# Kernel optimization log

Measured on AMD Instinct MI355X. Metric: run time of the kernel, lower is better.

Reference implementation:

```python
import jax, jax.numpy as jnp
import numpy as np

ANCHOR_RADIUS = 5.0


def setup_inputs() -> dict:
    key = jax.random.key(0)
    k1, k2, k3 = jax.random.split(key, 3)
    B, N, E, S = 4, 1024, 32, 2
    embedding = jax.random.normal(k1, (B, N, E), dtype=jnp.float32)
    abs_coords = 10.0 * jax.random.normal(k2, (B, N, S), dtype=jnp.float32)
    patch_mask = jax.random.bernoulli(k3, 0.5, (B, N, N))  # bool [B,N,N]
    return {"embedding": embedding, "abs_coords": abs_coords, "patch_mask": patch_mask}


def reference(embedding, abs_coords, patch_mask):
    B, N, E = embedding.shape
    # pairwise coordinate and embedding differences
    coord_diff = abs_coords[:, :, None, :] - abs_coords[:, None, :, :]   # [B,N,N,2]
    diff = embedding[:, :, None, :] - embedding[:, None, :, :]           # [B,N,N,E]
    diff = diff.at[..., :2].add(coord_diff)
    ssq = jnp.sum(diff * diff, axis=-1)                                   # [B,N,N]
    # safe sqrt: zero grad at zero distance (matches torch norm subgradient)
    dist = jnp.where(ssq == 0, 0.0, jnp.sqrt(jnp.where(ssq == 0, 1.0, ssq)))
    sim = 1.0 - jax.nn.sigmoid(dist * 5.0 / ANCHOR_RADIUS - 5.0)          # [B,N,N]

    # negatives: sim with positive-pair mask and diagonal set to -inf
    eye = jnp.eye(N, dtype=bool)
    neg_mask = patch_mask | eye
    neg_masked = jnp.where(neg_mask, -jnp.inf, sim)                       # [B,N,N]
    lse_neg = jax.scipy.special.logsumexp(neg_masked, axis=-1)            # [B,N]

    # For each positive pair (b,i,j) with patch_mask[b,i,j]:
    #   logits = [sim[b,i,j], neg_masked[b,i,:]] ; CE target=0 ->
    #   loss_contrib = logaddexp(sim[b,i,j], lse_neg[b,i]) - sim[b,i,j]
    lse_tot = jnp.logaddexp(sim, lse_neg[:, :, None])                     # [B,N,N]
    loss = jnp.sum(jnp.where(patch_mask, lse_tot - sim, 0.0))
    return loss
```

## Files before the change

### kernel.cpp

```cpp
#include <hip/hip_runtime.h>

#define BBATCH 4
#define NN 1024
#define EE 32

typedef short v8s __attribute__((ext_vector_type(8)));
typedef float v4f __attribute__((ext_vector_type(4)));

__device__ __forceinline__ unsigned short f32_to_bf16(float v) {
    unsigned u = __builtin_bit_cast(unsigned, v);
    u += 0x7fffu + ((u >> 16) & 1u);
    return (unsigned short)(u >> 16);
}

__global__ __launch_bounds__(1024) void fused_kernel(
    const float* __restrict__ emb, const float* __restrict__ coords,
    const int* __restrict__ mask, float* __restrict__ out)
{
    const int bid = blockIdx.x;
    const int is = bid & 63;
    const int b  = bid >> 6;
    const int tid  = threadIdx.x;
    const int wave = tid >> 6, lane = tid & 63;
    const int m = lane & 15, q = lane >> 4;

    __shared__ unsigned short yh_s[NN * EE];
    __shared__ float nrm_s[NN];
    __shared__ float sums_w[16][16];
    __shared__ float total_s[16];
    __shared__ float wred[16];

    const float4* src4 = (const float4*)(emb + (size_t)b * NN * EE);
    const float*  crdb = coords + (size_t)b * NN * 2;
    #pragma unroll
    for (int w = 0; w < 8; ++w) {
        const int g  = w * 1024 + tid;
        const int r  = g >> 3, qq = g & 7;
        float4 v = src4[g];
        if (qq == 0) { v.x += crdb[r * 2 + 0]; v.y += crdb[r * 2 + 1]; }
        ushort4 h;
        h.x = f32_to_bf16(v.x); h.y = f32_to_bf16(v.y);
        h.z = f32_to_bf16(v.z); h.w = f32_to_bf16(v.w);
        ((ushort4*)yh_s)[r * 8 + (qq ^ (r & 7))] = h;
        float p = v.x * v.x + v.y * v.y + v.z * v.z + v.w * v.w;
        #pragma unroll
        for (int off = 1; off < 8; off <<= 1) p += __shfl_xor(p, off, 64);
        if (qq == 0) nrm_s[r] = p;
    }
    __syncthreads();

    const int i0 = is * 16;
    const v8s af = *(const v8s*)(yh_s + ((i0 + m) * EE) + ((q ^ (m & 7)) * 8));
    float ni[4];
    #pragma unroll
    for (int r = 0; r < 4; ++r) ni[r] = nrm_s[i0 + q * 4 + r];

    const int jbase = wave * 64;
    float    ex[4][4];
    float    s[4] = {0.f, 0.f, 0.f, 0.f};
    unsigned mbits = 0u;

    #pragma unroll
    for (int t = 0; t < 4; ++t) {
        const int j0 = jbase + t * 16;
        const v8s bf = *(const v8s*)(yh_s + ((j0 + m) * EE) + ((q ^ (m & 7)) * 8));
        const float njv = nrm_s[j0 + m];
        int mk[4];
        #pragma unroll
        for (int r = 0; r < 4; ++r)
            mk[r] = mask[((size_t)(b * NN + i0 + q * 4 + r) << 10) + j0 + m];
        v4f d = __builtin_amdgcn_mfma_f32_16x16x32_bf16(af, bf, (v4f){0,0,0,0}, 0, 0, 0);
        #pragma unroll
        for (int r = 0; r < 4; ++r) {
            float ssq  = fmaxf(ni[r] + njv - 2.f * d[r], 0.f);
            float dist = sqrtf(ssq);
            float sm   = 1.f / (1.f + __expf(dist - 5.f));
            const float e = __expf(mk[r] != 0 ? -sm : sm);
            ex[t][r] = e;
            bool negm = (mk[r] != 0) || (i0 + q * 4 + r == j0 + m);
            s[r] += negm ? 0.f : e;
            if (mk[r] != 0) mbits |= 1u << (t * 4 + r);
        }
    }

    #pragma unroll
    for (int r = 0; r < 4; ++r) {
        float v = s[r];
        #pragma unroll
        for (int off = 8; off > 0; off >>= 1) v += __shfl_down(v, off, 16);
        if (m == 0) sums_w[wave][q * 4 + r] = v;
    }
    __syncthreads();
    if (tid < 16) {
        float tot = 0.f;
        #pragma unroll
        for (int w = 0; w < 16; ++w) tot += sums_w[w][tid];
        total_s[tid] = tot;
    }
    __syncthreads();

    float tot[4];
    #pragma unroll
    for (int r = 0; r < 4; ++r) tot[r] = total_s[q * 4 + r];
    float acc = 0.f;
    #pragma unroll
    for (int t = 0; t < 4; ++t)
        #pragma unroll
        for (int r = 0; r < 4; ++r)
            if ((mbits >> (t * 4 + r)) & 1u)
                acc += __logf(fmaf(tot[r], ex[t][r], 1.f));

    #pragma unroll
    for (int off = 32; off > 0; off >>= 1) acc += __shfl_down(acc, off, 64);
    if (lane == 0) wred[wave] = acc;
    __syncthreads();
    if (tid == 0) {
        float a = 0.f;
        #pragma unroll
        for (int w = 0; w < 16; ++w) a += wred[w];
        atomicAdd(out, a);
    }
}

extern "C" void kernel_launch(void* const* d_in, const int* in_sizes, int n_in,
                              void* d_out, int out_size, void* d_ws, size_t ws_size,
                              hipStream_t stream) {
    const float* emb    = (const float*)d_in[0];
    const float* coords = (const float*)d_in[1];
    const int*   mask   = (const int*)d_in[2];
    float*       out    = (float*)d_out;

    hipMemsetAsync(out, 0, sizeof(float), stream);
    fused_kernel<<<BBATCH * (NN / 16), 1024, 0, stream>>>(emb, coords, mask, out);
}
```

Before: 80.13 us.

## Hoist bf16 conversion and norms into a separate prep kernel

Moves the per-block conversion of embeddings (plus coords) to bf16 and the row-norm computation into a standalone prep kernel writing to workspace, so it is done once per batch instead of once per block. The main kernel now reads bf16 rows and norms directly from global memory and no longer needs 64KB of LDS or a block-wide barrier before compute. Also uses native sqrt/rcp intrinsics and a branchless masked log accumulation. Adds a second kernel launch and global-memory reads of the operands in place of LDS reads.

```diff
diff --git a/kernel.cpp b/kernel.cpp
--- a/kernel.cpp
+++ b/kernel.cpp
@@ -13,8 +13,26 @@
     return (unsigned short)(u >> 16);
 }
 
+__global__ __launch_bounds__(256) void prep_kernel(
+    const float* __restrict__ emb, const float* __restrict__ coords,
+    unsigned short* __restrict__ ybf, float* __restrict__ nrm)
+{
+    const int g  = blockIdx.x * 256 + threadIdx.x;
+    const int r  = g >> 3, qq = g & 7;
+    float4 v = ((const float4*)emb)[g];
+    if (qq == 0) { v.x += coords[r * 2 + 0]; v.y += coords[r * 2 + 1]; }
+    ushort4 h;
+    h.x = f32_to_bf16(v.x); h.y = f32_to_bf16(v.y);
+    h.z = f32_to_bf16(v.z); h.w = f32_to_bf16(v.w);
+    ((ushort4*)ybf)[g] = h;
+    float p = v.x * v.x + v.y * v.y + v.z * v.z + v.w * v.w;
+    #pragma unroll
+    for (int off = 1; off < 8; off <<= 1) p += __shfl_xor(p, off, 64);
+    if (qq == 0) nrm[r] = p;
+}
+
 __global__ __launch_bounds__(1024) void fused_kernel(
-    const float* __restrict__ emb, const float* __restrict__ coords,
+    const unsigned short* __restrict__ ybf, const float* __restrict__ nrm,
     const int* __restrict__ mask, float* __restrict__ out)
 {
     const int bid = blockIdx.x;
@@ -24,36 +42,19 @@
     const int wave = tid >> 6, lane = tid & 63;
     const int m = lane & 15, q = lane >> 4;
 
-    __shared__ unsigned short yh_s[NN * EE];
-    __shared__ float nrm_s[NN];
     __shared__ float sums_w[16][16];
     __shared__ float total_s[16];
     __shared__ float wred[16];
 
-    const float4* src4 = (const float4*)(emb + (size_t)b * NN * EE);
-    const float*  crdb = coords + (size_t)b * NN * 2;
-    #pragma unroll
-    for (int w = 0; w < 8; ++w) {
-        const int g  = w * 1024 + tid;
-        const int r  = g >> 3, qq = g & 7;
-        float4 v = src4[g];
-        if (qq == 0) { v.x += crdb[r * 2 + 0]; v.y += crdb[r * 2 + 1]; }
-        ushort4 h;
-        h.x = f32_to_bf16(v.x); h.y = f32_to_bf16(v.y);
-        h.z = f32_to_bf16(v.z); h.w = f32_to_bf16(v.w);
-        ((ushort4*)yh_s)[r * 8 + (qq ^ (r & 7))] = h;
-        float p = v.x * v.x + v.y * v.y + v.z * v.z + v.w * v.w;
-        #pragma unroll
-        for (int off = 1; off < 8; off <<= 1) p += __shfl_xor(p, off, 64);
-        if (qq == 0) nrm_s[r] = p;
-    }
-    __syncthreads();
+    const unsigned short* Y  = ybf + (size_t)b * NN * EE;
+    const float*          NR = nrm + b * NN;
+    const int i0   = is * 16;
+    const int irow = i0 + q * 4;
 
-    const int i0 = is * 16;
-    const v8s af = *(const v8s*)(yh_s + ((i0 + m) * EE) + ((q ^ (m & 7)) * 8));
+    const v8s af = *(const v8s*)(Y + (i0 + m) * EE + q * 8);
     float ni[4];
     #pragma unroll
-    for (int r = 0; r < 4; ++r) ni[r] = nrm_s[i0 + q * 4 + r];
+    for (int r = 0; r < 4; ++r) ni[r] = NR[irow + r];
 
     const int jbase = wave * 64;
     float    ex[4][4];
@@ -63,21 +64,22 @@
     #pragma unroll
     for (int t = 0; t < 4; ++t) {
         const int j0 = jbase + t * 16;
-        const v8s bf = *(const v8s*)(yh_s + ((j0 + m) * EE) + ((q ^ (m & 7)) * 8));
-        const float njv = nrm_s[j0 + m];
+        const v8s bfv = *(const v8s*)(Y + (j0 + m) * EE + q * 8);
+        const float njv = NR[j0 + m];
         int mk[4];
         #pragma unroll
         for (int r = 0; r < 4; ++r)
-            mk[r] = mask[((size_t)(b * NN + i0 + q * 4 + r) << 10) + j0 + m];
-        v4f d = __builtin_amdgcn_mfma_f32_16x16x32_bf16(af, bf, (v4f){0,0,0,0}, 0, 0, 0);
+            mk[r] = mask[((size_t)(b * NN + irow + r) << 10) + j0 + m];
+        v4f d = __builtin_amdgcn_mfma_f32_16x16x32_bf16(af, bfv, (v4f){0,0,0,0}, 0, 0, 0);
         #pragma unroll
         for (int r = 0; r < 4; ++r) {
-            float ssq  = fmaxf(ni[r] + njv - 2.f * d[r], 0.f);
-            float dist = sqrtf(ssq);
-            float sm   = 1.f / (1.f + __expf(dist - 5.f));
+            float nn   = ni[r] + njv;
+            float ssq  = fmaxf(fmaf(-2.f, d[r], nn), 0.f);
+            float dist = __builtin_amdgcn_sqrtf(ssq);
+            float sm   = __builtin_amdgcn_rcpf(1.f + __expf(dist - 5.f));
             const float e = __expf(mk[r] != 0 ? -sm : sm);
             ex[t][r] = e;
-            bool negm = (mk[r] != 0) || (i0 + q * 4 + r == j0 + m);
+            bool negm = (mk[r] != 0) || (irow + r == j0 + m);
             s[r] += negm ? 0.f : e;
             if (mk[r] != 0) mbits |= 1u << (t * 4 + r);
         }
@@ -106,9 +108,10 @@
     #pragma unroll
     for (int t = 0; t < 4; ++t)
         #pragma unroll
-        for (int r = 0; r < 4; ++r)
-            if ((mbits >> (t * 4 + r)) & 1u)
-                acc += __logf(fmaf(tot[r], ex[t][r], 1.f));
+        for (int r = 0; r < 4; ++r) {
+            float lg = __logf(fmaf(tot[r], ex[t][r], 1.f));
+            acc += ((mbits >> (t * 4 + r)) & 1u) ? lg : 0.f;
+        }
 
     #pragma unroll
     for (int off = 32; off > 0; off >>= 1) acc += __shfl_down(acc, off, 64);
@@ -130,6 +133,10 @@
     const int*   mask   = (const int*)d_in[2];
     float*       out    = (float*)d_out;
 
+    unsigned short* ybf = (unsigned short*)d_ws;
+    float*          nrv = (float*)((char*)d_ws + BBATCH * NN * EE * 2);
+
     hipMemsetAsync(out, 0, sizeof(float), stream);
-    fused_kernel<<<BBATCH * (NN / 16), 1024, 0, stream>>>(emb, coords, mask, out);
+    prep_kernel<<<(BBATCH * NN * EE / 4) / 256, 256, 0, stream>>>(emb, coords, ybf, nrv);
+    fused_kernel<<<BBATCH * (NN / 16), 1024, 0, stream>>>(ybf, nrv, mask, out);
 }
```

After: 79.20 us. About the same (-1.2%).
